# Kernel tuning notes

Hardware: AMD Instinct MI355X
Metric: run time of the kernel (lower is better)

The kernel has to match this reference:

```python
import jax, jax.numpy as jnp
import numpy as np

DIM = 1024
NUM_HEADS = 16
HEAD_DIM = DIM // NUM_HEADS
SCALE = HEAD_DIM ** -0.5
B, N = 2, 2048


def setup_inputs() -> dict:
    key = jax.random.key(0)
    k_x, k_qkv, k_prjw, k_prjb = jax.random.split(key, 4)
    # nn.Linear(dim, 3*dim, bias=False): weight [3*dim, dim]
    s = 1.0 / np.sqrt(DIM)
    return {
        "x": jax.random.normal(k_x, (B, N, DIM), dtype=jnp.float32),
        "w_qkv": jax.random.uniform(k_qkv, (3 * DIM, DIM), jnp.float32, -s, s),
        "w_prj": jax.random.uniform(k_prjw, (DIM, DIM), jnp.float32, -s, s),
        "b_prj": jax.random.uniform(k_prjb, (DIM,), jnp.float32, -s, s),
    }


def reference(x, w_qkv, w_prj, b_prj):
    Bb, Nn, C = x.shape
    qkv = jnp.einsum("bnc,dc->bnd", x, w_qkv)            # [B,N,3C]
    qkv = qkv.reshape(Bb, Nn, 3, NUM_HEADS, HEAD_DIM)
    qkv = jnp.transpose(qkv, (2, 0, 3, 1, 4))            # [3,B,H,N,hd]
    q, k, v = qkv[0], qkv[1], qkv[2]
    attn = jnp.einsum("bhqd,bhkd->bhqk", q, k) * SCALE   # [B,H,N,N]
    attn = jax.nn.softmax(attn, axis=-1)
    out = jnp.einsum("bhqk,bhkd->bhqd", attn, v)         # [B,H,N,hd]
    out = jnp.transpose(out, (0, 2, 1, 3)).reshape(Bb, Nn, C)
    # dropout layers are identity at eval / p=0
    return jnp.einsum("bnc,dc->bnd", out, w_prj) + b_prj
```

## Files before the change

### kernel.cpp

```cpp
#include <hip/hip_runtime.h>

typedef unsigned short u16;
typedef unsigned int u32;
typedef __attribute__((ext_vector_type(8))) short s16x8;
typedef __attribute__((ext_vector_type(4))) float f32x4;

#define DIM    1024
#define NHEADS 16
#define HD     64
#define NSEQ   2048
#define QKVN   3072

__device__ __forceinline__ u16 f2bf(float f) {
  u32 u = __float_as_uint(f);
  u += 0x7FFF + ((u >> 16) & 1);
  return (u16)(u >> 16);
}

__device__ __forceinline__ float vexp2(float x) {
  float r;
  asm volatile("v_exp_f32 %0, %1" : "=v"(r) : "v"(x));
  return r;
}

__device__ __forceinline__ void async16(const u16* g, u16* l) {
  __builtin_amdgcn_global_load_lds(
      (const __attribute__((address_space(1))) unsigned int*)g,
      (__attribute__((address_space(3))) unsigned int*)l, 16, 0, 0);
}

__global__ void cast_all(const float* __restrict__ x, const float* __restrict__ wq,
                         const float* __restrict__ wp, u16* __restrict__ xo,
                         u16* __restrict__ wqo, u16* __restrict__ wpo) {
  int i = blockIdx.x * 256 + threadIdx.x;
  const float4* src; u16* dst; int off;
  if (i < 1048576)      { src = (const float4*)x;  dst = xo;  off = i; }
  else if (i < 1835008) { src = (const float4*)wq; dst = wqo; off = i - 1048576; }
  else                  { src = (const float4*)wp; dst = wpo; off = i - 1835008; }
  float4 f = src[off];
  ushort4 o;
  o.x = f2bf(f.x); o.y = f2bf(f.y); o.z = f2bf(f.z); o.w = f2bf(f.w);
  ((ushort4*)dst)[off] = o;
}

template <bool FINAL>
__global__ __launch_bounds__(256, 3) void gemm_bt(
    const u16* __restrict__ A, const u16* __restrict__ Bw, u16* __restrict__ qkv,
    u16* __restrict__ vt, const float* __restrict__ bias, float* __restrict__ outp) {
  constexpr int K = 1024;
  constexpr int BM = FINAL ? 64 : 128;
  constexpr int MT = FINAL ? 64 : 32;
  constexpr int IT = FINAL ? 2 : 4;
  constexpr int ACALLS = BM / 8;
  constexpr int TCALLS = ACALLS + 16;
  constexpr int PW = TCALLS / 4;
  const int bm = blockIdx.x % MT;
  const int bn = blockIdx.x / MT;
  const int tid = threadIdx.x;
  const int wave = tid >> 6, lane = tid & 63;
  const int q4 = lane >> 4, l15 = lane & 15;
  const int wm = wave >> 1, wn = wave & 1;
  const int m0 = bm * BM, n0 = bn * 128;

  __shared__ alignas(16) u16 lsA[BM * 64];
  __shared__ alignas(16) u16 lsB[128 * 64];

  f32x4 acc[IT][4];
#pragma unroll
  for (int i = 0; i < IT; i++)
#pragma unroll
    for (int j = 0; j < 4; j++) acc[i][j] = (f32x4){0.f, 0.f, 0.f, 0.f};

  for (int k0 = 0; k0 < K; k0 += 64) {
    __syncthreads();
#pragma unroll
    for (int j = 0; j < PW; ++j) {
      int t = wave * PW + j;
      if (t < ACALLS) {
        int lin = t * 64 + lane;
        int r = lin >> 3, cs = lin & 7, c = cs ^ (r & 7);
        async16(A + (size_t)(m0 + r) * K + k0 + c * 8, lsA + t * 512);
      } else {
        int tb = t - ACALLS;
        int lin = tb * 64 + lane;
        int r = lin >> 3, cs = lin & 7, c = cs ^ (r & 7);
        async16(Bw + (size_t)(n0 + r) * K + k0 + c * 8, lsB + tb * 512);
      }
    }
    __syncthreads();
#pragma unroll
    for (int kc = 0; kc < 2; ++kc) {
      s16x8 af[IT], bfr[4];
#pragma unroll
      for (int i = 0; i < IT; ++i) {
        int r = wm * (IT * 16) + i * 16 + l15;
        int c = (kc * 4 + q4) ^ (r & 7);
        af[i] = *(const s16x8*)(lsA + r * 64 + c * 8);
      }
#pragma unroll
      for (int j = 0; j < 4; ++j) {
        int r = wn * 64 + j * 16 + l15;
        int c = (kc * 4 + q4) ^ (r & 7);
        bfr[j] = *(const s16x8*)(lsB + r * 64 + c * 8);
      }
#pragma unroll
      for (int i = 0; i < IT; ++i)
#pragma unroll
        for (int j = 0; j < 4; ++j)
          acc[i][j] = __builtin_amdgcn_mfma_f32_16x16x32_bf16(af[i], bfr[j], acc[i][j], 0, 0, 0);
    }
  }

#pragma unroll
  for (int i = 0; i < IT; i++) {
#pragma unroll
    for (int j = 0; j < 4; j++) {
      int n = n0 + wn * 64 + j * 16 + l15;
      int mb = m0 + wm * (IT * 16) + i * 16 + q4 * 4;
      if (FINAL) {
#pragma unroll
        for (int r = 0; r < 4; r++)
          outp[(size_t)(mb + r) * DIM + n] = acc[i][j][r] + bias[n];
      } else if (n < 2048) {
#pragma unroll
        for (int r = 0; r < 4; r++)
          qkv[(size_t)(mb + r) * QKVN + n] = f2bf(acc[i][j][r]);
      } else {
        int b = mb >> 11, tok = mb & 2047;
        int h = (n >> 6) & 15, hd = n & 63;
        ushort4 pk;
        pk.x = f2bf(acc[i][j][0]); pk.y = f2bf(acc[i][j][1]);
        pk.z = f2bf(acc[i][j][2]); pk.w = f2bf(acc[i][j][3]);
        *(ushort4*)(vt + ((size_t)((b * NHEADS + h) * HD + hd)) * NSEQ + tok) = pk;
      }
    }
  }
}

__global__ __launch_bounds__(256, 6) void attn_kernel(const u16* __restrict__ qkv,
                                                      const u16* __restrict__ vt,
                                                      u16* __restrict__ aout) {
  const int blk = blockIdx.x;
  const int bh = blk & 31, qt = blk >> 5;
  const int b = bh >> 4, h = bh & 15;
  const int tid = threadIdx.x;
  const int wave = tid >> 6, lane = tid & 63;
  const int q4 = lane >> 4, l15 = lane & 15;

  __shared__ alignas(16) u16 lsK[64 * 64];
  __shared__ alignas(16) u16 lsV[64 * 64];
  __shared__ alignas(16) u16 lsP[4][16 * 72];

  const float QSCALE = 0.18033688011112042f;
  s16x8 aq[2];
#pragma unroll
  for (int kc = 0; kc < 2; ++kc) {
    int row = b * NSEQ + qt * 64 + wave * 16 + l15;
    uint4 d = *(const uint4*)(qkv + (size_t)row * QKVN + h * HD + kc * 32 + q4 * 8);
    u32 w[4] = {d.x, d.y, d.z, d.w};
    s16x8 f;
#pragma unroll
    for (int j = 0; j < 8; ++j) {
      u16 u = (u16)(w[j >> 1] >> ((j & 1) * 16));
      float v = __uint_as_float(((u32)u) << 16) * QSCALE;
      f[j] = (short)f2bf(v);
    }
    aq[kc] = f;
  }

  f32x4 o[4];
  float lsum[4] = {0.f, 0.f, 0.f, 0.f};
#pragma unroll
  for (int ht = 0; ht < 4; ++ht) o[ht] = (f32x4){0.f, 0.f, 0.f, 0.f};

  for (int kt = 0; kt < 32; ++kt) {
    __syncthreads();
#pragma unroll
    for (int j = 0; j < 2; ++j) {
      int t = wave * 2 + j;
      int lin = t * 64 + lane;
      int r = lin >> 3, c = (lin & 7) ^ (r & 7);
      async16(qkv + (size_t)(b * NSEQ + kt * 64 + r) * QKVN + DIM + h * HD + c * 8,
              lsK + t * 512);
      async16(vt + (size_t)(bh * HD + r) * NSEQ + kt * 64 + c * 8,
              lsV + t * 512);
    }
    __syncthreads();

    f32x4 s[4];
#pragma unroll
    for (int ct = 0; ct < 4; ++ct) s[ct] = (f32x4){0.f, 0.f, 0.f, 0.f};
#pragma unroll
    for (int kc = 0; kc < 2; ++kc) {
#pragma unroll
      for (int ct = 0; ct < 4; ++ct) {
        int r = ct * 16 + l15;
        int c = (kc * 4 + q4) ^ (r & 7);
        s16x8 bk = *(const s16x8*)(lsK + r * 64 + c * 8);
        s[ct] = __builtin_amdgcn_mfma_f32_16x16x32_bf16(aq[kc], bk, s[ct], 0, 0, 0);
      }
    }

#pragma unroll
    for (int ct = 0; ct < 4; ++ct)
#pragma unroll
      for (int r = 0; r < 4; ++r) {
        u32 u = __float_as_uint(vexp2(s[ct][r]));
        lsum[r] += __uint_as_float(u & 0xffff0000u);
        lsP[wave][(q4 * 4 + r) * 72 + ct * 16 + l15] = (u16)(u >> 16);
      }

#pragma unroll
    for (int kc = 0; kc < 2; ++kc) {
      s16x8 pa = *(const s16x8*)(lsP[wave] + l15 * 72 + kc * 32 + q4 * 8);
#pragma unroll
      for (int ht = 0; ht < 4; ++ht) {
        int r = ht * 16 + l15;
        int c = (kc * 4 + q4) ^ (r & 7);
        s16x8 vb = *(const s16x8*)(lsV + r * 64 + c * 8);
        o[ht] = __builtin_amdgcn_mfma_f32_16x16x32_bf16(pa, vb, o[ht], 0, 0, 0);
      }
    }
  }

#pragma unroll
  for (int off = 1; off < 16; off <<= 1)
#pragma unroll
    for (int r = 0; r < 4; ++r) lsum[r] += __shfl_xor(lsum[r], off, 64);
  float inv[4];
#pragma unroll
  for (int r = 0; r < 4; ++r) inv[r] = 1.0f / lsum[r];

#pragma unroll
  for (int ht = 0; ht < 4; ++ht)
#pragma unroll
    for (int r = 0; r < 4; ++r) {
      int n = qt * 64 + wave * 16 + q4 * 4 + r;
      int col = h * HD + ht * 16 + l15;
      aout[(size_t)(b * NSEQ + n) * DIM + col] = f2bf(o[ht][r] * inv[r]);
    }
}

extern "C" void kernel_launch(void* const* d_in, const int* in_sizes, int n_in,
                              void* d_out, int out_size, void* d_ws, size_t ws_size,
                              hipStream_t stream) {
  const float* x     = (const float*)d_in[0];
  const float* w_qkv = (const float*)d_in[1];
  const float* w_prj = (const float*)d_in[2];
  const float* b_prj = (const float*)d_in[3];
  float* out = (float*)d_out;

  char* ws = (char*)d_ws;
  u16* x_bf    = (u16*)(ws);
  u16* wqkv_bf = (u16*)(ws + (size_t)(8u << 20));
  u16* wprj_bf = (u16*)(ws + (size_t)(14u << 20));
  u16* qkv     = (u16*)(ws + (size_t)(16u << 20));
  u16* vt      = (u16*)(ws + (size_t)(40u << 20));
  u16* aout    = (u16*)(ws + (size_t)(48u << 20));

  cast_all<<<8192, 256, 0, stream>>>(x, w_qkv, w_prj, x_bf, wqkv_bf, wprj_bf);
  gemm_bt<false><<<32 * 24, 256, 0, stream>>>(x_bf, wqkv_bf, qkv, vt, nullptr, nullptr);
  attn_kernel<<<1024, 256, 0, stream>>>(qkv, vt, aout);
  gemm_bt<true><<<64 * 8, 256, 0, stream>>>(aout, wprj_bf, nullptr, nullptr, b_prj, out);
}
```

Before: 189.4 us.

## Double-buffer K/V tiles and process 128 query rows per attention block

```diff
diff --git a/kernel.cpp b/kernel.cpp
--- a/kernel.cpp
+++ b/kernel.cpp
@@ -137,7 +137,7 @@
   }
 }
 
-__global__ __launch_bounds__(256, 6) void attn_kernel(const u16* __restrict__ qkv,
+__global__ __launch_bounds__(256, 2) void attn_kernel(const u16* __restrict__ qkv,
                                                       const u16* __restrict__ vt,
                                                       u16* __restrict__ aout) {
   const int blk = blockIdx.x;
@@ -147,98 +147,116 @@
   const int wave = tid >> 6, lane = tid & 63;
   const int q4 = lane >> 4, l15 = lane & 15;
 
-  __shared__ alignas(16) u16 lsK[64 * 64];
-  __shared__ alignas(16) u16 lsV[64 * 64];
+  __shared__ alignas(16) u16 lsK[2][64 * 64];
+  __shared__ alignas(16) u16 lsV[2][64 * 64];
   __shared__ alignas(16) u16 lsP[4][16 * 72];
 
   const float QSCALE = 0.18033688011112042f;
-  s16x8 aq[2];
-#pragma unroll
-  for (int kc = 0; kc < 2; ++kc) {
-    int row = b * NSEQ + qt * 64 + wave * 16 + l15;
-    uint4 d = *(const uint4*)(qkv + (size_t)row * QKVN + h * HD + kc * 32 + q4 * 8);
-    u32 w[4] = {d.x, d.y, d.z, d.w};
-    s16x8 f;
-#pragma unroll
-    for (int j = 0; j < 8; ++j) {
-      u16 u = (u16)(w[j >> 1] >> ((j & 1) * 16));
-      float v = __uint_as_float(((u32)u) << 16) * QSCALE;
-      f[j] = (short)f2bf(v);
-    }
-    aq[kc] = f;
-  }
-
-  f32x4 o[4];
-  float lsum[4] = {0.f, 0.f, 0.f, 0.f};
-#pragma unroll
-  for (int ht = 0; ht < 4; ++ht) o[ht] = (f32x4){0.f, 0.f, 0.f, 0.f};
-
-  for (int kt = 0; kt < 32; ++kt) {
-    __syncthreads();
+  s16x8 aq[2][2];
+#pragma unroll
+  for (int rt = 0; rt < 2; ++rt)
+#pragma unroll
+    for (int kc = 0; kc < 2; ++kc) {
+      int row = b * NSEQ + qt * 128 + wave * 32 + rt * 16 + l15;
+      uint4 d = *(const uint4*)(qkv + (size_t)row * QKVN + h * HD + kc * 32 + q4 * 8);
+      u32 w[4] = {d.x, d.y, d.z, d.w};
+      s16x8 f;
+#pragma unroll
+      for (int j = 0; j < 8; ++j) {
+        u16 u = (u16)(w[j >> 1] >> ((j & 1) * 16));
+        float v = __uint_as_float(((u32)u) << 16) * QSCALE;
+        f[j] = (short)f2bf(v);
+      }
+      aq[rt][kc] = f;
+    }
+
+  f32x4 o[2][4];
+  float lsum[2][4] = {{0.f, 0.f, 0.f, 0.f}, {0.f, 0.f, 0.f, 0.f}};
+#pragma unroll
+  for (int rt = 0; rt < 2; ++rt)
+#pragma unroll
+    for (int ht = 0; ht < 4; ++ht) o[rt][ht] = (f32x4){0.f, 0.f, 0.f, 0.f};
+
+  auto stage = [&](int kt, int buf) {
 #pragma unroll
     for (int j = 0; j < 2; ++j) {
       int t = wave * 2 + j;
       int lin = t * 64 + lane;
       int r = lin >> 3, c = (lin & 7) ^ (r & 7);
       async16(qkv + (size_t)(b * NSEQ + kt * 64 + r) * QKVN + DIM + h * HD + c * 8,
-              lsK + t * 512);
+              lsK[buf] + t * 512);
       async16(vt + (size_t)(bh * HD + r) * NSEQ + kt * 64 + c * 8,
-              lsV + t * 512);
-    }
+              lsV[buf] + t * 512);
+    }
+  };
+
+  stage(0, 0);
+
+  for (int kt = 0; kt < 32; ++kt) {
+    const int buf = kt & 1;
     __syncthreads();
-
-    f32x4 s[4];
-#pragma unroll
-    for (int ct = 0; ct < 4; ++ct) s[ct] = (f32x4){0.f, 0.f, 0.f, 0.f};
-#pragma unroll
-    for (int kc = 0; kc < 2; ++kc) {
-#pragma unroll
-      for (int ct = 0; ct < 4; ++ct) {
-        int r = ct * 16 + l15;
-        int c = (kc * 4 + q4) ^ (r & 7);
-        s16x8 bk = *(const s16x8*)(lsK + r * 64 + c * 8);
-        s[ct] = __builtin_amdgcn_mfma_f32_16x16x32_bf16(aq[kc], bk, s[ct], 0, 0, 0);
-      }
-    }
-
-#pragma unroll
-    for (int ct = 0; ct < 4; ++ct)
+    if (kt + 1 < 32) stage(kt + 1, buf ^ 1);
+
+#pragma unroll
+    for (int rt = 0; rt < 2; ++rt) {
+      f32x4 s[4];
+#pragma unroll
+      for (int ct = 0; ct < 4; ++ct) s[ct] = (f32x4){0.f, 0.f, 0.f, 0.f};
+#pragma unroll
+      for (int kc = 0; kc < 2; ++kc) {
+#pragma unroll
+        for (int ct = 0; ct < 4; ++ct) {
+          int r = ct * 16 + l15;
+          int c = (kc * 4 + q4) ^ (r & 7);
+          s16x8 bk = *(const s16x8*)(lsK[buf] + r * 64 + c * 8);
+          s[ct] = __builtin_amdgcn_mfma_f32_16x16x32_bf16(aq[rt][kc], bk, s[ct], 0, 0, 0);
+        }
+      }
+
+#pragma unroll
+      for (int ct = 0; ct < 4; ++ct)
+#pragma unroll
+        for (int r = 0; r < 4; ++r) {
+          u32 u = __float_as_uint(vexp2(s[ct][r]));
+          lsum[rt][r] += __uint_as_float(u & 0xffff0000u);
+          lsP[wave][(q4 * 4 + r) * 72 + ct * 16 + l15] = (u16)(u >> 16);
+        }
+
+#pragma unroll
+      for (int kc = 0; kc < 2; ++kc) {
+        s16x8 pa = *(const s16x8*)(lsP[wave] + l15 * 72 + kc * 32 + q4 * 8);
+#pragma unroll
+        for (int ht = 0; ht < 4; ++ht) {
+          int r = ht * 16 + l15;
+          int c = (kc * 4 + q4) ^ (r & 7);
+          s16x8 vb = *(const s16x8*)(lsV[buf] + r * 64 + c * 8);
+          o[rt][ht] = __builtin_amdgcn_mfma_f32_16x16x32_bf16(pa, vb, o[rt][ht], 0, 0, 0);
+        }
+      }
+    }
+  }
+
+#pragma unroll
+  for (int off = 1; off < 16; off <<= 1)
+#pragma unroll
+    for (int rt = 0; rt < 2; ++rt)
+#pragma unroll
+      for (int r = 0; r < 4; ++r) lsum[rt][r] += __shfl_xor(lsum[rt][r], off, 64);
+
+#pragma unroll
+  for (int rt = 0; rt < 2; ++rt) {
+    float inv[4];
+#pragma unroll
+    for (int r = 0; r < 4; ++r) inv[r] = 1.0f / lsum[rt][r];
+#pragma unroll
+    for (int ht = 0; ht < 4; ++ht)
 #pragma unroll
       for (int r = 0; r < 4; ++r) {
-        u32 u = __float_as_uint(vexp2(s[ct][r]));
-        lsum[r] += __uint_as_float(u & 0xffff0000u);
-        lsP[wave][(q4 * 4 + r) * 72 + ct * 16 + l15] = (u16)(u >> 16);
-      }
-
-#pragma unroll
-    for (int kc = 0; kc < 2; ++kc) {
-      s16x8 pa = *(const s16x8*)(lsP[wave] + l15 * 72 + kc * 32 + q4 * 8);
-#pragma unroll
-      for (int ht = 0; ht < 4; ++ht) {
-        int r = ht * 16 + l15;
-        int c = (kc * 4 + q4) ^ (r & 7);
-        s16x8 vb = *(const s16x8*)(lsV + r * 64 + c * 8);
-        o[ht] = __builtin_amdgcn_mfma_f32_16x16x32_bf16(pa, vb, o[ht], 0, 0, 0);
-      }
-    }
-  }
-
-#pragma unroll
-  for (int off = 1; off < 16; off <<= 1)
-#pragma unroll
-    for (int r = 0; r < 4; ++r) lsum[r] += __shfl_xor(lsum[r], off, 64);
-  float inv[4];
-#pragma unroll
-  for (int r = 0; r < 4; ++r) inv[r] = 1.0f / lsum[r];
-
-#pragma unroll
-  for (int ht = 0; ht < 4; ++ht)
-#pragma unroll
-    for (int r = 0; r < 4; ++r) {
-      int n = qt * 64 + wave * 16 + q4 * 4 + r;
-      int col = h * HD + ht * 16 + l15;
-      aout[(size_t)(b * NSEQ + n) * DIM + col] = f2bf(o[ht][r] * inv[r]);
-    }
+        int n = qt * 128 + wave * 32 + rt * 16 + q4 * 4 + r;
+        int col = h * HD + ht * 16 + l15;
+        aout[(size_t)(b * NSEQ + n) * DIM + col] = f2bf(o[rt][ht][r] * inv[r]);
+      }
+  }
 }
 
 extern "C" void kernel_launch(void* const* d_in, const int* in_sizes, int n_in,
@@ -260,6 +278,6 @@
 
   cast_all<<<8192, 256, 0, stream>>>(x, w_qkv, w_prj, x_bf, wqkv_bf, wprj_bf);
   gemm_bt<false><<<32 * 24, 256, 0, stream>>>(x_bf, wqkv_bf, qkv, vt, nullptr, nullptr);
-  attn_kernel<<<1024, 256, 0, stream>>>(qkv, vt, aout);
+  attn_kernel<<<512, 256, 0, stream>>>(qkv, vt, aout);
   gemm_bt<true><<<64 * 8, 256, 0, stream>>>(aout, wprj_bf, nullptr, nullptr, b_prj, out);
 }
```

Result: no change. 189.4 us (+0.0%).
